# Performance work log

Measured on AMD Instinct MI355X. Metric: run time of the kernel, lower is better.

Reference implementation:

```python
import jax, jax.numpy as jnp
import numpy as np

IN_DIM = 1024
OUT_DIM = 1024
NUM_HEADS = 16
DEPTH = IN_DIM // NUM_HEADS  # 64


def setup_inputs() -> dict:
    key = jax.random.key(0)
    ks = jax.random.split(key, 11)
    B, S = 8, 1024  # S must equal IN_DIM (reshape constraint in original module)
    s_in = 1.0 / np.sqrt(IN_DIM)
    return {
        "query": jax.random.normal(ks[0], (B, S, IN_DIM), jnp.float32),
        "key": jax.random.normal(ks[1], (B, S, IN_DIM), jnp.float32),
        "value": jax.random.normal(ks[2], (B, S, IN_DIM), jnp.float32),
        "Wq": jax.random.normal(ks[3], (IN_DIM, IN_DIM), jnp.float32) * s_in,
        "bq": jnp.zeros((IN_DIM,), jnp.float32),
        "Wk": jax.random.normal(ks[4], (IN_DIM, IN_DIM), jnp.float32) * s_in,
        "bk": jnp.zeros((IN_DIM,), jnp.float32),
        "Wv": jax.random.normal(ks[5], (IN_DIM, IN_DIM), jnp.float32) * s_in,
        "bv": jnp.zeros((IN_DIM,), jnp.float32),
        "Wo": jax.random.normal(ks[6], (OUT_DIM, IN_DIM), jnp.float32) * s_in,
        "bo": jnp.zeros((OUT_DIM,), jnp.float32),
    }


def reference(query, key, value, Wq, bq, Wk, bk, Wv, bv, Wo, bo):
    B, S, D = query.shape
    H, P = NUM_HEADS, DEPTH

    def split_heads(x):
        # (B,S,D) -> (B,S,H,P) -> transpose last two dims -> (B,S,P,H)
        return x.reshape(B, S, H, P).swapaxes(-1, -2)

    Q = split_heads(query @ Wq.T + bq)   # (B,S,P,H)
    K = split_heads(key @ Wk.T + bk)     # (B,S,P,H)
    V = split_heads(value @ Wv.T + bv)   # (B,S,P,H)

    scale = jnp.sqrt(jnp.float32(P))
    # scores over the depth axis, per (batch, token): (B,S,P,P)
    scores = jnp.einsum('bsph,bsqh->bspq', Q, K) / scale
    # original uses softmax over dim=0 (the batch axis) - reproduce faithfully
    attn = jax.nn.softmax(scores, axis=0)
    out = jnp.einsum('bspq,bsqh->bsph', attn, V)   # (B,S,P,H)
    # transpose(-1,-2) -> (B,S,H,P), reshape to (B,S,S) (requires H*P == S)
    out = out.swapaxes(-1, -2).reshape(B, S, S)
    out = out @ Wo.T + bo                           # (B,S,OUT_DIM)
    return jax.nn.sigmoid(out)
```

## Files before the change

### kernel.cpp

```cpp
#include <hip/hip_runtime.h>


using short8  = __attribute__((ext_vector_type(8))) short;
using floatx4 = __attribute__((ext_vector_type(4))) float;

__device__ __forceinline__ float bf2f(unsigned short u) {
    return __uint_as_float(((unsigned)u) << 16);
}
__device__ __forceinline__ unsigned short f2bf(float f) {
    unsigned u = __float_as_uint(f);
    u += 0x7fffu + ((u >> 16) & 1u);
    return (unsigned short)(u >> 16);
}
__device__ __forceinline__ unsigned pack_trunc(float f0, float f1) {
    return __builtin_amdgcn_perm(__float_as_uint(f1), __float_as_uint(f0), 0x07060302u);
}
__device__ __forceinline__ void async_ld16(const void* g, void* l) {
    __builtin_amdgcn_global_load_lds(
        (const __attribute__((address_space(1))) unsigned int*)g,
        (__attribute__((address_space(3))) unsigned int*)l, 16, 0, 0);
}

__global__ __launch_bounds__(256) void convert_weights(
    const float* __restrict__ w0, const float* __restrict__ w1,
    const float* __restrict__ w2, const float* __restrict__ w3,
    unsigned short* __restrict__ dst)
{
    const float* srcs[4] = {w0, w1, w2, w3};
    const float* src = srcs[blockIdx.y];
    unsigned short* d = dst + (size_t)blockIdx.y * (1024u * 1024u);
    const size_t i = ((size_t)blockIdx.x * 256 + threadIdx.x) * 8;
    float4 a = *(const float4*)(src + i);
    float4 b = *(const float4*)(src + i + 4);
    uint4 o;
    o.x = ((unsigned)f2bf(a.y) << 16) | f2bf(a.x);
    o.y = ((unsigned)f2bf(a.w) << 16) | f2bf(a.z);
    o.z = ((unsigned)f2bf(b.y) << 16) | f2bf(b.x);
    o.w = ((unsigned)f2bf(b.w) << 16) | f2bf(b.z);
    *(uint4*)(d + i) = o;
}

template<bool AF32, bool SIG>
__global__ __launch_bounds__(256) void gemm128(
    const void* __restrict__ A0, const void* __restrict__ A1, const void* __restrict__ A2,
    const unsigned short* __restrict__ W0, const unsigned short* __restrict__ W1,
    const unsigned short* __restrict__ W2,
    const float* __restrict__ b0, const float* __restrict__ b1, const float* __restrict__ b2,
    void* __restrict__ C0, void* __restrict__ C1, void* __restrict__ C2)
{
    const int z = blockIdx.z;
    const void* Ap = (z == 0) ? A0 : (z == 1) ? A1 : A2;
    const unsigned short* W = (z == 0) ? W0 : (z == 1) ? W1 : W2;
    const float* bias = (z == 0) ? b0 : (z == 1) ? b1 : b2;
    void* Cp = (z == 0) ? C0 : (z == 1) ? C1 : C2;

    constexpr int Kd = 1024, Nd = 1024;
    const int t = threadIdx.x;
    const int w = t >> 6, lane = t & 63;
    const int l15 = lane & 15, quad = lane >> 4;
    const int blockM = blockIdx.x * 128;
    const int blockN = blockIdx.y * 128;
    const int wy = w >> 1, wx = w & 1;

    __shared__ unsigned short Bs[128 * 32];
    constexpr int ABYTES = AF32 ? (128 * 32 * 4) : (128 * 32 * 2);
    __shared__ __align__(16) unsigned char AsRaw[ABYTES];
    float* AsF = (float*)AsRaw;
    unsigned short* AsB = (unsigned short*)AsRaw;

    const int br  = lane >> 2;
    const int bg  = (lane & 3) ^ (br & 3);
    const unsigned short* Bsrc0 = W + (size_t)(blockN + w * 32 + br) * Kd + bg * 8;
    const unsigned short* Bsrc1 = Bsrc0 + (size_t)16 * Kd;
    unsigned short* Bdst0 = &Bs[(w * 2 + 0) * 512];
    unsigned short* Bdst1 = &Bs[(w * 2 + 1) * 512];

    const int ar = lane >> 3;
    const int ag = (lane & 7) ^ (ar & 7);
    const float* AsrcF[4];
    float* AdstF[4];
    const unsigned short* AsrcB0 = nullptr; const unsigned short* AsrcB1 = nullptr;
    unsigned short* AdstB0 = nullptr; unsigned short* AdstB1 = nullptr;
    if (AF32) {
        #pragma unroll
        for (int j = 0; j < 4; ++j) {
            AsrcF[j] = (const float*)Ap + (size_t)(blockM + w * 32 + j * 8 + ar) * Kd + ag * 4;
            AdstF[j] = AsF + (w * 4 + j) * 256;
        }
    } else {
        AsrcB0 = (const unsigned short*)Ap + (size_t)(blockM + w * 32 + br) * Kd + bg * 8;
        AsrcB1 = AsrcB0 + (size_t)16 * Kd;
        AdstB0 = &AsB[(w * 2 + 0) * 512];
        AdstB1 = &AsB[(w * 2 + 1) * 512];
    }

    floatx4 acc[4][4] = {};

    for (int k0 = 0; k0 < Kd; k0 += 32) {
        if (AF32) {
            #pragma unroll
            for (int j = 0; j < 4; ++j) async_ld16(AsrcF[j] + k0, AdstF[j]);
        } else {
            async_ld16(AsrcB0 + k0, AdstB0);
            async_ld16(AsrcB1 + k0, AdstB1);
        }
        async_ld16(Bsrc0 + k0, Bdst0);
        async_ld16(Bsrc1 + k0, Bdst1);
        __syncthreads();

        short8 af[4], bfr[4];
        #pragma unroll
        for (int mt = 0; mt < 4; ++mt) {
            const int row = wy * 64 + mt * 16 + l15;
            if (AF32) {
                const int r7 = l15 & 7;
                const float* ap = AsF + row * 32;
                float4 lo = *(const float4*)(ap + (((quad * 2 + 0) ^ r7) * 4));
                float4 hi = *(const float4*)(ap + (((quad * 2 + 1) ^ r7) * 4));
                union { unsigned u[4]; short8 s; } cv;
                cv.u[0] = pack_trunc(lo.x, lo.y);
                cv.u[1] = pack_trunc(lo.z, lo.w);
                cv.u[2] = pack_trunc(hi.x, hi.y);
                cv.u[3] = pack_trunc(hi.z, hi.w);
                af[mt] = cv.s;
            } else {
                af[mt] = *(const short8*)&AsB[row * 32 + (quad ^ (l15 & 3)) * 8];
            }
        }
        #pragma unroll
        for (int nt = 0; nt < 4; ++nt) {
            const int row = wx * 64 + nt * 16 + l15;
            bfr[nt] = *(const short8*)&Bs[row * 32 + (quad ^ (l15 & 3)) * 8];
        }
        #pragma unroll
        for (int mt = 0; mt < 4; ++mt)
            #pragma unroll
            for (int nt = 0; nt < 4; ++nt)
                acc[mt][nt] = __builtin_amdgcn_mfma_f32_16x16x32_bf16(af[mt], bfr[nt], acc[mt][nt], 0, 0, 0);
        __syncthreads();
    }

    #pragma unroll
    for (int nt = 0; nt < 4; ++nt) {
        const int col = blockN + wx * 64 + nt * 16 + l15;
        const float bv = bias[col];
        #pragma unroll
        for (int mt = 0; mt < 4; ++mt) {
            const int row = blockM + wy * 64 + mt * 16 + quad * 4;
            #pragma unroll
            for (int r = 0; r < 4; ++r) {
                float v = acc[mt][nt][r] + bv;
                if (SIG) {
                    v = 1.0f / (1.0f + __expf(-v));
                    ((float*)Cp)[(size_t)(row + r) * Nd + col] = v;
                } else {
                    ((unsigned short*)Cp)[(size_t)(row + r) * Nd + col] = f2bf(v);
                }
            }
        }
    }
}

__device__ __forceinline__ float dot4q(const float* qf, ushort4 k) {
    return qf[0] * bf2f(k.x) + qf[1] * bf2f(k.y) + qf[2] * bf2f(k.z) + qf[3] * bf2f(k.w);
}
__device__ __forceinline__ void axpy4(float* o, float w, ushort4 v) {
    o[0] += w * bf2f(v.x); o[1] += w * bf2f(v.y); o[2] += w * bf2f(v.z); o[3] += w * bf2f(v.w);
}

__global__ __launch_bounds__(512) void attn_kernel(
    const unsigned short* __restrict__ Q,
    const unsigned short* __restrict__ Kt,
    const unsigned short* __restrict__ Vt,
    unsigned short* __restrict__ O2)
{
    constexpr int QS = 20;
    constexpr int PB = 64 * QS + 4;
    __shared__ unsigned short Kl[8 * PB];
    __shared__ unsigned short Vl[8 * PB];

    const int s = blockIdx.x;
    const int t = threadIdx.x;

    {
        const int b8 = t >> 6, lq = t & 63;
        const unsigned short* Ks = Kt + ((size_t)b8 * 1024 + s) * 1024;
        const unsigned short* Vs = Vt + ((size_t)b8 * 1024 + s) * 1024;
        unsigned* kd = (unsigned*)&Kl[b8 * PB + lq * QS];
        unsigned* vd = (unsigned*)&Vl[b8 * PB + lq * QS];
        #pragma unroll
        for (int w2 = 0; w2 < 8; ++w2) {
            unsigned klo = Ks[(2 * w2) * 64 + lq], khi = Ks[(2 * w2 + 1) * 64 + lq];
            kd[w2] = klo | (khi << 16);
            unsigned vlo = Vs[(2 * w2) * 64 + lq], vhi = Vs[(2 * w2 + 1) * 64 + lq];
            vd[w2] = vlo | (vhi << 16);
        }
    }
    __syncthreads();

    const int b = t & 7;
    const int p = t >> 3;
    const size_t qbase = ((size_t)b * 1024 + s) * 1024 + p;

    float qf[16], o[16];
    #pragma unroll
    for (int h = 0; h < 16; ++h) { qf[h] = bf2f(Q[qbase + (size_t)h * 64]); o[h] = 0.0f; }

    const unsigned short* kp = &Kl[b * PB];
    const unsigned short* vp = &Vl[b * PB];

    for (int q = 0; q < 64; ++q) {
        const int off = q * QS;
        float sc = dot4q(qf + 0,  *(const ushort4*)&kp[off + 0])
                 + dot4q(qf + 4,  *(const ushort4*)&kp[off + 4])
                 + dot4q(qf + 8,  *(const ushort4*)&kp[off + 8])
                 + dot4q(qf + 12, *(const ushort4*)&kp[off + 12]);
        float e = __expf(sc * 0.125f);
        float d = e;
        d += __shfl_xor(d, 1);
        d += __shfl_xor(d, 2);
        d += __shfl_xor(d, 4);
        const float wgt = e * __builtin_amdgcn_rcpf(d);
        axpy4(o + 0,  wgt, *(const ushort4*)&vp[off + 0]);
        axpy4(o + 4,  wgt, *(const ushort4*)&vp[off + 4]);
        axpy4(o + 8,  wgt, *(const ushort4*)&vp[off + 8]);
        axpy4(o + 12, wgt, *(const ushort4*)&vp[off + 12]);
    }

    #pragma unroll
    for (int h = 0; h < 16; ++h)
        O2[qbase + (size_t)h * 64] = f2bf(o[h]);
}

extern "C" void kernel_launch(void* const* d_in, const int* in_sizes, int n_in,
                              void* d_out, int out_size, void* d_ws, size_t ws_size,
                              hipStream_t stream) {
    const float* query = (const float*)d_in[0];
    const float* key_  = (const float*)d_in[1];
    const float* value = (const float*)d_in[2];
    const float* Wq = (const float*)d_in[3];
    const float* bq = (const float*)d_in[4];
    const float* Wk = (const float*)d_in[5];
    const float* bk = (const float*)d_in[6];
    const float* Wv = (const float*)d_in[7];
    const float* bv = (const float*)d_in[8];
    const float* Wo = (const float*)d_in[9];
    const float* bo = (const float*)d_in[10];

    const size_t WN = (size_t)1024 * 1024;
    const size_t MN = (size_t)8192 * 1024;

    unsigned short* Wbf = (unsigned short*)d_ws;
    unsigned short* Wq_bf = Wbf;
    unsigned short* Wk_bf = Wbf + WN;
    unsigned short* Wv_bf = Wbf + 2 * WN;
    unsigned short* Wo_bf = Wbf + 3 * WN;
    unsigned short* Qb = Wbf + 4 * WN;
    unsigned short* Kb = Qb + MN;
    unsigned short* Vb = Kb + MN;
    unsigned short* O2 = Qb;

    convert_weights<<<dim3(512, 4), dim3(256), 0, stream>>>(Wq, Wk, Wv, Wo, Wbf);

    gemm128<true, false><<<dim3(64, 8, 3), dim3(256), 0, stream>>>(
        query, key_, value, Wq_bf, Wk_bf, Wv_bf, bq, bk, bv, Qb, Kb, Vb);

    attn_kernel<<<dim3(1024), dim3(512), 0, stream>>>(Qb, Kb, Vb, O2);

    gemm128<false, true><<<dim3(64, 8, 1), dim3(256), 0, stream>>>(
        O2, O2, O2, Wo_bf, Wo_bf, Wo_bf, bo, bo, bo, d_out, d_out, d_out);
}
```

Before: 333.6 us.

## Pre-convert activations to bf16 and stage Q/output through LDS in attention

When workspace is large enough, the fp32 query/key/value inputs are first converted to bf16 in a separate pass so the QKV GEMM can use its bf16 A-operand path. The attention kernel now loads Q into shared memory with the same coalesced pattern used for K and V, and writes the output through LDS to make the global stores coalesced, replacing strided per-thread accesses. The extra conversion pass adds a full read and write of the activations plus an extra launch, and the attention kernel uses more LDS and an extra barrier.

```diff
diff --git a/kernel.cpp b/kernel.cpp
--- a/kernel.cpp
+++ b/kernel.cpp
@@ -21,15 +21,7 @@
         (__attribute__((address_space(3))) unsigned int*)l, 16, 0, 0);
 }
 
-__global__ __launch_bounds__(256) void convert_weights(
-    const float* __restrict__ w0, const float* __restrict__ w1,
-    const float* __restrict__ w2, const float* __restrict__ w3,
-    unsigned short* __restrict__ dst)
-{
-    const float* srcs[4] = {w0, w1, w2, w3};
-    const float* src = srcs[blockIdx.y];
-    unsigned short* d = dst + (size_t)blockIdx.y * (1024u * 1024u);
-    const size_t i = ((size_t)blockIdx.x * 256 + threadIdx.x) * 8;
+__device__ __forceinline__ void conv8(const float* src, unsigned short* d, size_t i) {
     float4 a = *(const float4*)(src + i);
     float4 b = *(const float4*)(src + i + 4);
     uint4 o;
@@ -38,6 +30,25 @@
     o.z = ((unsigned)f2bf(b.y) << 16) | f2bf(b.x);
     o.w = ((unsigned)f2bf(b.w) << 16) | f2bf(b.z);
     *(uint4*)(d + i) = o;
+}
+
+__global__ __launch_bounds__(256) void convert_weights(
+    const float* __restrict__ w0, const float* __restrict__ w1,
+    const float* __restrict__ w2, const float* __restrict__ w3,
+    unsigned short* __restrict__ dst)
+{
+    const float* srcs[4] = {w0, w1, w2, w3};
+    conv8(srcs[blockIdx.y], dst + (size_t)blockIdx.y * (1024u * 1024u),
+          ((size_t)blockIdx.x * 256 + threadIdx.x) * 8);
+}
+
+__global__ __launch_bounds__(256) void convert_acts(
+    const float* __restrict__ a0, const float* __restrict__ a1,
+    const float* __restrict__ a2, unsigned short* __restrict__ dst)
+{
+    const float* srcs[3] = {a0, a1, a2};
+    conv8(srcs[blockIdx.y], dst + (size_t)blockIdx.y * ((size_t)8192 * 1024),
+          ((size_t)blockIdx.x * 256 + threadIdx.x) * 8);
 }
 
 template<bool AF32, bool SIG>
@@ -178,33 +189,47 @@
     constexpr int PB = 64 * QS + 4;
     __shared__ unsigned short Kl[8 * PB];
     __shared__ unsigned short Vl[8 * PB];
+    __shared__ unsigned short Ql[8 * PB];
 
     const int s = blockIdx.x;
     const int t = threadIdx.x;
+    const int b8 = t >> 6, lq = t & 63;
 
     {
-        const int b8 = t >> 6, lq = t & 63;
-        const unsigned short* Ks = Kt + ((size_t)b8 * 1024 + s) * 1024;
-        const unsigned short* Vs = Vt + ((size_t)b8 * 1024 + s) * 1024;
+        const size_t gbase = ((size_t)b8 * 1024 + s) * 1024;
+        const unsigned short* Ks = Kt + gbase;
+        const unsigned short* Vs = Vt + gbase;
+        const unsigned short* Qs = Q  + gbase;
         unsigned* kd = (unsigned*)&Kl[b8 * PB + lq * QS];
         unsigned* vd = (unsigned*)&Vl[b8 * PB + lq * QS];
+        unsigned* qd = (unsigned*)&Ql[b8 * PB + lq * QS];
         #pragma unroll
         for (int w2 = 0; w2 < 8; ++w2) {
             unsigned klo = Ks[(2 * w2) * 64 + lq], khi = Ks[(2 * w2 + 1) * 64 + lq];
             kd[w2] = klo | (khi << 16);
             unsigned vlo = Vs[(2 * w2) * 64 + lq], vhi = Vs[(2 * w2 + 1) * 64 + lq];
             vd[w2] = vlo | (vhi << 16);
+            unsigned qlo = Qs[(2 * w2) * 64 + lq], qhi = Qs[(2 * w2 + 1) * 64 + lq];
+            qd[w2] = qlo | (qhi << 16);
         }
     }
     __syncthreads();
 
     const int b = t & 7;
     const int p = t >> 3;
-    const size_t qbase = ((size_t)b * 1024 + s) * 1024 + p;
 
     float qf[16], o[16];
-    #pragma unroll
-    for (int h = 0; h < 16; ++h) { qf[h] = bf2f(Q[qbase + (size_t)h * 64]); o[h] = 0.0f; }
+    {
+        const unsigned short* qp = &Ql[b * PB + p * QS];
+        #pragma unroll
+        for (int h4 = 0; h4 < 4; ++h4) {
+            ushort4 qv = *(const ushort4*)&qp[h4 * 4];
+            qf[h4 * 4 + 0] = bf2f(qv.x); qf[h4 * 4 + 1] = bf2f(qv.y);
+            qf[h4 * 4 + 2] = bf2f(qv.z); qf[h4 * 4 + 3] = bf2f(qv.w);
+        }
+        #pragma unroll
+        for (int h = 0; h < 16; ++h) o[h] = 0.0f;
+    }
 
     const unsigned short* kp = &Kl[b * PB];
     const unsigned short* vp = &Vl[b * PB];
@@ -227,9 +252,24 @@
         axpy4(o + 12, wgt, *(const ushort4*)&vp[off + 12]);
     }
 
-    #pragma unroll
-    for (int h = 0; h < 16; ++h)
-        O2[qbase + (size_t)h * 64] = f2bf(o[h]);
+    {
+        unsigned* od = (unsigned*)&Ql[b * PB + p * QS];
+        #pragma unroll
+        for (int w2 = 0; w2 < 8; ++w2)
+            od[w2] = ((unsigned)f2bf(o[2 * w2 + 1]) << 16) | f2bf(o[2 * w2]);
+    }
+    __syncthreads();
+
+    {
+        const size_t gbase = ((size_t)b8 * 1024 + s) * 1024;
+        const unsigned* qd = (const unsigned*)&Ql[b8 * PB + lq * QS];
+        #pragma unroll
+        for (int w2 = 0; w2 < 8; ++w2) {
+            unsigned v = qd[w2];
+            O2[gbase + (2 * w2) * 64 + lq]     = (unsigned short)(v & 0xffff);
+            O2[gbase + (2 * w2 + 1) * 64 + lq] = (unsigned short)(v >> 16);
+        }
+    }
 }
 
 extern "C" void kernel_launch(void* const* d_in, const int* in_sizes, int n_in,
@@ -255,16 +295,25 @@
     unsigned short* Wk_bf = Wbf + WN;
     unsigned short* Wv_bf = Wbf + 2 * WN;
     unsigned short* Wo_bf = Wbf + 3 * WN;
-    unsigned short* Qb = Wbf + 4 * WN;
-    unsigned short* Kb = Qb + MN;
-    unsigned short* Vb = Kb + MN;
+
+    convert_weights<<<dim3(512, 4), dim3(256), 0, stream>>>(Wq, Wk, Wv, Wo, Wbf);
+
+    const bool big = ws_size >= (4 * WN + 6 * MN) * sizeof(unsigned short);
+
+    unsigned short* Qb; unsigned short* Kb; unsigned short* Vb;
+    if (big) {
+        unsigned short* abf = Wbf + 4 * WN;
+        Qb = abf + 3 * MN; Kb = Qb + MN; Vb = Kb + MN;
+        convert_acts<<<dim3(4096, 3), dim3(256), 0, stream>>>(query, key_, value, abf);
+        gemm128<false, false><<<dim3(64, 8, 3), dim3(256), 0, stream>>>(
+            abf, abf + MN, abf + 2 * MN, Wq_bf, Wk_bf, Wv_bf, bq, bk, bv, Qb, Kb, Vb);
+    } else {
+        Qb = Wbf + 4 * WN; Kb = Qb + MN; Vb = Kb + MN;
+        gemm128<true, false><<<dim3(64, 8, 3), dim3(256), 0, stream>>>(
+            query, key_, value, Wq_bf, Wk_bf, Wv_bf, bq, bk, bv, Qb, Kb, Vb);
+    }
+
     unsigned short* O2 = Qb;
-
-    convert_weights<<<dim3(512, 4), dim3(256), 0, stream>>>(Wq, Wk, Wv, Wo, Wbf);
-
-    gemm128<true, false><<<dim3(64, 8, 3), dim3(256), 0, stream>>>(
-        query, key_, value, Wq_bf, Wk_bf, Wv_bf, bq, bk, bv, Qb, Kb, Vb);
-
     attn_kernel<<<dim3(1024), dim3(512), 0, stream>>>(Qb, Kb, Vb, O2);
 
     gemm128<false, true><<<dim3(64, 8, 1), dim3(256), 0, stream>>>(
```

Result: no change. 329.0 us (-1.4%).
